# Performance work log

Measured on AMD Instinct MI355X. Metric: run time of the kernel, lower is better.

The kernel has to match this reference:

```python
import jax, jax.numpy as jnp
import numpy as np

T, B, D, H, L = 64, 512, 1536, 1024, 4
DISCOUNT = 0.997
LAM = 0.95


def setup_inputs() -> dict:
    key = jax.random.key(0)
    ks = jax.random.split(key, 3 + L + 1)
    inp = {
        'feat': jax.random.normal(ks[0], (T, B, D), dtype=jnp.float32),
        'reward': jax.random.normal(ks[1], (T - 1, B), dtype=jnp.float32),
        'cont': jnp.ones((T, B), dtype=jnp.float32),
    }
    scale = 0.02
    dims = [D] + [H] * L
    for i in range(L):
        inp[f'W{i}'] = jax.random.normal(ks[3 + i], (dims[i], dims[i + 1]), dtype=jnp.float32) * scale
        inp[f'b{i}'] = jnp.zeros((dims[i + 1],), dtype=jnp.float32)
    inp['Wo'] = jax.random.normal(ks[3 + L], (H,), dtype=jnp.float32) * scale
    inp['bo'] = jnp.zeros((), dtype=jnp.float32)
    return inp


def reference(feat, reward, cont, W0, b0, W1, b1, W2, b2, W3, b3, Wo, bo):
    # Value-net MLP (mean of critic dist): [T, B, D] -> [T, B]
    h = feat
    for W, b in ((W0, b0), (W1, b1), (W2, b2), (W3, b3)):
        h = jax.nn.silu(h @ W + b)
    value = h @ Wo + bo  # [T, B]

    disc = cont[1:] * DISCOUNT                      # [T-1, B]
    deltas = reward + disc * value[1:] - value[:-1]  # [T-1, B]

    # GAE: adv_t = delta_t + disc_t * lambda * adv_{t+1}, adv_T = 0
    def step(adv_next, xs):
        delta, dl = xs
        adv = delta + dl * adv_next
        return adv, adv

    _, advs = jax.lax.scan(step, jnp.zeros_like(value[0]),
                           (deltas, disc * LAM), reverse=True)
    ret = advs + value[:-1]   # lambda-return target, [T-1, B]
    baseline = value[:-1]
    return ret, baseline
```

## Files before the change

kernel.cpp:

```cpp
#include <hip/hip_runtime.h>
#include <hip/hip_bf16.h>

#define T_DIM 64
#define B_DIM 512
#define D_DIM 1536
#define H_DIM 1024
#define M_DIM (T_DIM * B_DIM)
#define DISCOUNT 0.997f
#define LAM 0.95f

#define BM 128
#define BN 128
#define BK 64
#define TILES_M 256
#define TILES_N 8
#define N_XCD 8

typedef __bf16 bf16x8 __attribute__((ext_vector_type(8)));
typedef float  f32x4  __attribute__((ext_vector_type(4)));

__device__ __forceinline__ void async_load16(const void* g, void* l) {
    __builtin_amdgcn_global_load_lds(
        (const __attribute__((address_space(1))) void*)g,
        (__attribute__((address_space(3))) void*)l,
        16, 0, 0);
}

__device__ __forceinline__ unsigned short f2bf_raw(float f) {
    __hip_bfloat16 h = __float2bfloat16(f);
    return *reinterpret_cast<unsigned short*>(&h);
}

__global__ __launch_bounds__(256) void cvt_bf16_kernel(
    const float* __restrict__ x, __hip_bfloat16* __restrict__ y, long n4) {
    long i = (long)blockIdx.x * blockDim.x + threadIdx.x;
    if (i >= n4) return;
    float4 v = reinterpret_cast<const float4*>(x)[i];
    ushort4 o;
    o.x = f2bf_raw(v.x);
    o.y = f2bf_raw(v.y);
    o.z = f2bf_raw(v.z);
    o.w = f2bf_raw(v.w);
    reinterpret_cast<ushort4*>(y)[i] = o;
}

__global__ __launch_bounds__(256) void transpose_cvt_all_kernel(
    const float* __restrict__ W0, const float* __restrict__ W1,
    const float* __restrict__ W2, const float* __restrict__ W3,
    __hip_bfloat16* __restrict__ T0, __hip_bfloat16* __restrict__ T1,
    __hip_bfloat16* __restrict__ T2, __hip_bfloat16* __restrict__ T3) {
    __shared__ float tile[32][33];
    int z = blockIdx.z;
    const float* W;
    __hip_bfloat16* Tt;
    int K;
    if (z == 0)      { W = W0; Tt = T0; K = D_DIM; }
    else if (z == 1) { W = W1; Tt = T1; K = H_DIM; }
    else if (z == 2) { W = W2; Tt = T2; K = H_DIM; }
    else             { W = W3; Tt = T3; K = H_DIM; }
    int k0 = blockIdx.x * 32, n0 = blockIdx.y * 32;
    if (k0 >= K) return;
    int tx = threadIdx.x, ty = threadIdx.y;
    #pragma unroll
    for (int r = ty; r < 32; r += 8)
        tile[r][tx] = W[(size_t)(k0 + r) * H_DIM + n0 + tx];
    __syncthreads();
    #pragma unroll
    for (int r = ty; r < 32; r += 8)
        Tt[(size_t)(n0 + r) * K + k0 + tx] = __float2bfloat16(tile[tx][r]);
}

__global__ __launch_bounds__(256) void gemm_silu_kernel(
    const __hip_bfloat16* __restrict__ A,
    const __hip_bfloat16* __restrict__ Bt,
    const float* __restrict__ bias,
    __hip_bfloat16* __restrict__ C,
    int K) {

    __shared__ alignas(16) __hip_bfloat16 As[BM * BK];
    __shared__ alignas(16) __hip_bfloat16 Bs[BN * BK];

    const int tid  = threadIdx.x;
    const int wave = tid >> 6;
    const int lane = tid & 63;
    const int sub  = lane >> 3;
    const int quad = lane >> 4;
    const int r16  = lane & 15;
    const int wm   = wave & 1;
    const int wn   = wave >> 1;

    const int l     = blockIdx.x;
    const int xcd   = l & (N_XCD - 1);
    const int local = l >> 3;
    const int tn    = local & (TILES_N - 1);
    const int tm    = (xcd << 5) | (local >> 3);
    const int m0 = tm * BM;
    const int n0 = tn * BN;

    const int scol = (((lane & 7) ^ sub) << 3);

    f32x4 acc[4][4];
    #pragma unroll
    for (int i = 0; i < 4; ++i)
        #pragma unroll
        for (int j = 0; j < 4; ++j)
            acc[i][j] = (f32x4){0.f, 0.f, 0.f, 0.f};

    for (int k0 = 0; k0 < K; k0 += BK) {
        #pragma unroll
        for (int i = 0; i < 4; ++i) {
            int chunk = wave * 4 + i;
            const __hip_bfloat16* ga =
                A + (size_t)(m0 + chunk * 8 + sub) * K + k0 + scol;
            async_load16(ga, &As[chunk * 512]);
        }
        #pragma unroll
        for (int i = 0; i < 4; ++i) {
            int chunk = wave * 4 + i;
            const __hip_bfloat16* gb =
                Bt + (size_t)(n0 + chunk * 8 + sub) * K + k0 + scol;
            async_load16(gb, &Bs[chunk * 512]);
        }
        __syncthreads();

        #pragma unroll
        for (int kk = 0; kk < BK; kk += 32) {
            bf16x8 af[4], bf[4];
            #pragma unroll
            for (int i = 0; i < 4; ++i) {
                int m_l = wm * 64 + i * 16 + r16;
                int sa  = ((kk >> 3) + quad) ^ (m_l & 7);
                af[i] = *reinterpret_cast<const bf16x8*>(&As[m_l * BK + sa * 8]);
                int n_l = wn * 64 + i * 16 + r16;
                int sb  = ((kk >> 3) + quad) ^ (n_l & 7);
                bf[i] = *reinterpret_cast<const bf16x8*>(&Bs[n_l * BK + sb * 8]);
            }
            #pragma unroll
            for (int i = 0; i < 4; ++i)
                #pragma unroll
                for (int j = 0; j < 4; ++j)
                    acc[i][j] = __builtin_amdgcn_mfma_f32_16x16x32_bf16(
                        af[i], bf[j], acc[i][j], 0, 0, 0);
        }
        __syncthreads();
    }

    #pragma unroll
    for (int j = 0; j < 4; ++j) {
        int col = n0 + wn * 64 + j * 16 + r16;
        float bj = bias[col];
        #pragma unroll
        for (int i = 0; i < 4; ++i) {
            int row_base = m0 + wm * 64 + i * 16 + quad * 4;
            #pragma unroll
            for (int rr = 0; rr < 4; ++rr) {
                float v = acc[i][j][rr] + bj;
                float s = v / (1.f + __expf(-v));
                C[(size_t)(row_base + rr) * H_DIM + col] = __float2bfloat16(s);
            }
        }
    }
}

__global__ __launch_bounds__(256) void gemv_value_kernel(
    const __hip_bfloat16* __restrict__ H,
    const float* __restrict__ Wo,
    const float* __restrict__ bo_p,
    float* __restrict__ value, int M) {
    int wave = threadIdx.x >> 6, lane = threadIdx.x & 63;
    int row = blockIdx.x * 4 + wave;
    if (row >= M) return;
    const __hip_bfloat16* hrow = H + (size_t)row * H_DIM;
    float sum = 0.f;
    #pragma unroll
    for (int half = 0; half < 2; ++half) {
        int col = half * 512 + lane * 8;
        uint4 raw = *reinterpret_cast<const uint4*>(hrow + col);
        const __hip_bfloat16* hp = reinterpret_cast<const __hip_bfloat16*>(&raw);
        #pragma unroll
        for (int e = 0; e < 8; ++e)
            sum += __bfloat162float(hp[e]) * Wo[col + e];
    }
    #pragma unroll
    for (int off = 32; off > 0; off >>= 1)
        sum += __shfl_down(sum, off, 64);
    if (lane == 0) value[row] = sum + bo_p[0];
}

__global__ __launch_bounds__(64) void gae_kernel(
    const float* __restrict__ value,
    const float* __restrict__ reward,
    const float* __restrict__ cont,
    float* __restrict__ out) {
    int b = blockIdx.x * blockDim.x + threadIdx.x;
    if (b >= B_DIM) return;
    float adv = 0.f;
    float v_next = value[(T_DIM - 1) * B_DIM + b];
    for (int t = T_DIM - 2; t >= 0; --t) {
        float v_t  = value[t * B_DIM + b];
        float disc = cont[(t + 1) * B_DIM + b] * DISCOUNT;
        float delta = reward[t * B_DIM + b] + disc * v_next - v_t;
        adv = delta + disc * LAM * adv;
        out[t * B_DIM + b] = adv + v_t;
        out[(T_DIM - 1) * B_DIM + t * B_DIM + b] = v_t;
        v_next = v_t;
    }
}

extern "C" void kernel_launch(void* const* d_in, const int* in_sizes, int n_in,
                              void* d_out, int out_size, void* d_ws, size_t ws_size,
                              hipStream_t stream) {
    const float* feat   = (const float*)d_in[0];
    const float* reward = (const float*)d_in[1];
    const float* cont   = (const float*)d_in[2];
    const float* W[4]   = {(const float*)d_in[3], (const float*)d_in[5],
                           (const float*)d_in[7], (const float*)d_in[9]};
    const float* bias[4] = {(const float*)d_in[4], (const float*)d_in[6],
                            (const float*)d_in[8], (const float*)d_in[10]};
    const float* Wo = (const float*)d_in[11];
    const float* bo = (const float*)d_in[12];
    float* out = (float*)d_out;

    char* ws = (char*)d_ws;
    __hip_bfloat16* Xb = (__hip_bfloat16*)ws; ws += (size_t)M_DIM * D_DIM * 2;
    __hip_bfloat16* Ha = (__hip_bfloat16*)ws; ws += (size_t)M_DIM * H_DIM * 2;
    __hip_bfloat16* Hb = (__hip_bfloat16*)ws; ws += (size_t)M_DIM * H_DIM * 2;
    __hip_bfloat16* Wt0 = (__hip_bfloat16*)ws; ws += (size_t)H_DIM * D_DIM * 2;
    __hip_bfloat16* Wt1 = (__hip_bfloat16*)ws; ws += (size_t)H_DIM * H_DIM * 2;
    __hip_bfloat16* Wt2 = (__hip_bfloat16*)ws; ws += (size_t)H_DIM * H_DIM * 2;
    __hip_bfloat16* Wt3 = (__hip_bfloat16*)ws; ws += (size_t)H_DIM * H_DIM * 2;
    float* value = (float*)ws; ws += (size_t)M_DIM * 4;

    long n4 = (long)M_DIM * D_DIM / 4;
    cvt_bf16_kernel<<<(int)((n4 + 255) / 256), 256, 0, stream>>>(feat, Xb, n4);

    transpose_cvt_all_kernel<<<dim3(D_DIM / 32, H_DIM / 32, 4), dim3(32, 8), 0, stream>>>(
        W[0], W[1], W[2], W[3], Wt0, Wt1, Wt2, Wt3);

    const int nblocks = TILES_M * TILES_N;
    gemm_silu_kernel<<<nblocks, 256, 0, stream>>>(Xb, Wt0, bias[0], Ha, D_DIM);
    gemm_silu_kernel<<<nblocks, 256, 0, stream>>>(Ha, Wt1, bias[1], Hb, H_DIM);
    gemm_silu_kernel<<<nblocks, 256, 0, stream>>>(Hb, Wt2, bias[2], Ha, H_DIM);
    gemm_silu_kernel<<<nblocks, 256, 0, stream>>>(Ha, Wt3, bias[3], Hb, H_DIM);

    gemv_value_kernel<<<M_DIM / 4, 256, 0, stream>>>(Hb, Wo, bo, value, M_DIM);

    gae_kernel<<<8, 64, 0, stream>>>(value, reward, cont, out);
}
```

Before: 790.6 us.

## Double-buffer LDS tiles to overlap global loads with MFMA compute

Allocates two LDS buffers for the A and B tiles. The loads for the next K-slice are issued right after the barrier, so they overlap with the MFMA work on the current slice, and the trailing __syncthreads is removed. Global pointers are precomputed once and advanced each iteration. This doubles LDS use, which may reduce occupancy. The async writes into the other buffer rely on the top barrier to avoid a race.

```diff
diff --git a/kernel.cpp b/kernel.cpp
--- a/kernel.cpp
+++ b/kernel.cpp
@@ -77,8 +77,8 @@
     __hip_bfloat16* __restrict__ C,
     int K) {
 
-    __shared__ alignas(16) __hip_bfloat16 As[BM * BK];
-    __shared__ alignas(16) __hip_bfloat16 Bs[BN * BK];
+    __shared__ alignas(16) __hip_bfloat16 As[2][BM * BK];
+    __shared__ alignas(16) __hip_bfloat16 Bs[2][BN * BK];
 
     const int tid  = threadIdx.x;
     const int wave = tid >> 6;
@@ -99,6 +99,17 @@
 
     const int scol = (((lane & 7) ^ sub) << 3);
 
+    const __hip_bfloat16* ga[4];
+    const __hip_bfloat16* gb[4];
+    int ldsoff[4];
+    #pragma unroll
+    for (int i = 0; i < 4; ++i) {
+        int chunk = wave * 4 + i;
+        ga[i] = A  + (size_t)(m0 + chunk * 8 + sub) * K + scol;
+        gb[i] = Bt + (size_t)(n0 + chunk * 8 + sub) * K + scol;
+        ldsoff[i] = chunk * 512;
+    }
+
     f32x4 acc[4][4];
     #pragma unroll
     for (int i = 0; i < 4; ++i)
@@ -106,22 +117,24 @@
         for (int j = 0; j < 4; ++j)
             acc[i][j] = (f32x4){0.f, 0.f, 0.f, 0.f};
 
-    for (int k0 = 0; k0 < K; k0 += BK) {
-        #pragma unroll
-        for (int i = 0; i < 4; ++i) {
-            int chunk = wave * 4 + i;
-            const __hip_bfloat16* ga =
-                A + (size_t)(m0 + chunk * 8 + sub) * K + k0 + scol;
-            async_load16(ga, &As[chunk * 512]);
+    const int niter = K / BK;
+
+    #pragma unroll
+    for (int i = 0; i < 4; ++i) { async_load16(ga[i], &As[0][ldsoff[i]]); ga[i] += BK; }
+    #pragma unroll
+    for (int i = 0; i < 4; ++i) { async_load16(gb[i], &Bs[0][ldsoff[i]]); gb[i] += BK; }
+
+    int p = 0;
+    for (int k = 0; k < niter; ++k) {
+        asm volatile("s_waitcnt vmcnt(0)" ::: "memory");
+        asm volatile("s_barrier" ::: "memory");
+
+        if (k + 1 < niter) {
+            #pragma unroll
+            for (int i = 0; i < 4; ++i) { async_load16(ga[i], &As[p ^ 1][ldsoff[i]]); ga[i] += BK; }
+            #pragma unroll
+            for (int i = 0; i < 4; ++i) { async_load16(gb[i], &Bs[p ^ 1][ldsoff[i]]); gb[i] += BK; }
         }
-        #pragma unroll
-        for (int i = 0; i < 4; ++i) {
-            int chunk = wave * 4 + i;
-            const __hip_bfloat16* gb =
-                Bt + (size_t)(n0 + chunk * 8 + sub) * K + k0 + scol;
-            async_load16(gb, &Bs[chunk * 512]);
-        }
-        __syncthreads();
 
         #pragma unroll
         for (int kk = 0; kk < BK; kk += 32) {
@@ -130,10 +143,10 @@
             for (int i = 0; i < 4; ++i) {
                 int m_l = wm * 64 + i * 16 + r16;
                 int sa  = ((kk >> 3) + quad) ^ (m_l & 7);
-                af[i] = *reinterpret_cast<const bf16x8*>(&As[m_l * BK + sa * 8]);
+                af[i] = *reinterpret_cast<const bf16x8*>(&As[p][m_l * BK + sa * 8]);
                 int n_l = wn * 64 + i * 16 + r16;
                 int sb  = ((kk >> 3) + quad) ^ (n_l & 7);
-                bf[i] = *reinterpret_cast<const bf16x8*>(&Bs[n_l * BK + sb * 8]);
+                bf[i] = *reinterpret_cast<const bf16x8*>(&Bs[p][n_l * BK + sb * 8]);
             }
             #pragma unroll
             for (int i = 0; i < 4; ++i)
@@ -142,7 +155,7 @@
                     acc[i][j] = __builtin_amdgcn_mfma_f32_16x16x32_bf16(
                         af[i], bf[j], acc[i][j], 0, 0, 0);
         }
-        __syncthreads();
+        p ^= 1;
     }
 
     #pragma unroll
```

Result: faster. 758.3 us (-4.1%).
